# Kernel optimization log

Measured on AMD Instinct MI355X. Metric: run time of the kernel, lower is better.

The kernel has to match this reference:

```python
import jax, jax.numpy as jnp
import numpy as np

K = 512
U = 2
TEMP_BERN = 0.67
TEMP_CAT = 0.67
EULER = 0.5772156649015329
EPS = 1e-8
UEPS = 1e-6


def setup_inputs() -> dict:
    key = jax.random.key(0)
    ks = jax.random.split(key, 3)
    B, D = 16384, 1024
    inputs = jax.random.normal(ks[0], (B, D), jnp.float32)
    # glorot-normal-ish init for mW
    mW = jax.random.normal(ks[1], (D, K * U), jnp.float32) * jnp.sqrt(2.0 / (D + K * U))
    sW = jnp.full((D, K * U), -5.0, jnp.float32)
    conc1 = jnp.full((K,), 2.0, jnp.float32)
    conc0 = jnp.full((K,), 0.5453, jnp.float32)
    t_pi = jax.random.uniform(ks[2], (D, K), jnp.float32, 4.0, 5.0)
    biases = jnp.full((K * U,), 0.1, jnp.float32)
    return {"inputs": inputs, "mW": mW, "sW": sW, "conc1": conc1,
            "conc0": conc0, "t_pi": t_pi, "biases": biases}


def _uniform(k, shape):
    return jax.random.uniform(k, shape, jnp.float32, UEPS, 1.0 - UEPS)


def reference(inputs, mW, sW, conc1, conc0, t_pi, biases):
    rk = jax.random.split(jax.random.key(42), 4)

    # --- reparameterized weights W = mW + eps * softplus(sW) ---
    sW_sp = jax.nn.softplus(sW)
    eps = jax.lax.stop_gradient(jax.random.normal(rk[0], mW.shape, jnp.float32))
    W = mW + eps * sW_sp
    kl_weights = -0.5 * jnp.mean(2.0 * sW_sp - jnp.square(mW) - jnp.square(sW_sp) + 1.0)
    layer_loss = kl_weights / 60000.0

    # --- IBP: relaxed Bernoulli sample of t_pi ([D, K]) ---
    u = _uniform(rk[1], t_pi.shape)
    logistic = jnp.log(u) - jnp.log1p(-u)
    z_sample = jax.nn.sigmoid((t_pi + logistic) / TEMP_BERN)  # bin_concrete_sample
    z = jnp.tile(z_sample, (1, U))  # [D, K*U], column order u*K+k (as in TF code)

    # Kumaraswamy stick-breaking prior: cumprod along axis 0 (TF default)
    a_sp = jax.nn.softplus(conc1)  # [K]
    b_sp = jax.nn.softplus(conc0)  # [K]
    uk = _uniform(rk[2], t_pi.shape)
    q_u = jnp.power(1.0 - jnp.power(uk, 1.0 / b_sp), 1.0 / a_sp)  # kumaraswamy_sample
    prior_pi = jnp.cumprod(q_u, axis=0)
    q = jax.nn.sigmoid(t_pi)
    kl_z = jnp.sum(q * (jnp.log(q + EPS) - jnp.log(prior_pi + EPS)))

    # KL(Kumaraswamy(a,b) || Beta(1,1)); (beta-1) series term vanishes
    kl_sticks = jnp.sum(((a_sp - 1.0) / a_sp) * (-EULER - jax.scipy.special.digamma(b_sp) - 1.0 / b_sp)
                        + jnp.log(a_sp * b_sp + EPS) - (b_sp - 1.0) / b_sp)
    layer_loss = layer_loss + kl_sticks + kl_z

    W = z * W
    out = inputs @ W + biases  # [B, K*U]

    # --- LWTA activation via Gumbel-softmax over U competitors ---
    logits = out.reshape(-1, K, U)  # [B, K, U]
    g = -jnp.log(-jnp.log(_uniform(rk[3], logits.shape)))
    xi = jax.nn.softmax((logits + g) / TEMP_CAT, axis=-1)  # concrete_sample
    out_act = (logits * xi).reshape(out.shape)
    q_xi = jax.nn.softmax(logits, axis=-1)
    kl_xi = jnp.mean(jnp.sum(q_xi * (jnp.log(q_xi + EPS) - jnp.log(1.0 / U)), axis=1))
    layer_loss = layer_loss + kl_xi

    return out_act, layer_loss
```

## Files before the change

kernel.cpp:

```cpp
#include <hip/hip_runtime.h>
#include <stdint.h>
#include <math.h>

#define B_N   16384
#define D_N   1024
#define K_N   512
#define KU_N  1024
#define EPS_F 1e-8f
#define TEMP  0.67f
#define EULERC 0.5772156649015329f

#define HEPS  524288
#define HU    262144
#define HG    8388608

typedef uint32_t u32;
typedef __attribute__((ext_vector_type(4))) float f32x4;
typedef __attribute__((ext_vector_type(8))) __bf16 bf16x8;

#define TF_ROT(x, r) (((x) << (r)) | ((x) >> (32 - (r))))

__host__ __device__ static inline void threefry2x32(u32 k0, u32 k1,
                                                    u32 x0, u32 x1,
                                                    u32* o0, u32* o1) {
  u32 ks2 = k0 ^ k1 ^ 0x1BD11BDAu;
  x0 += k0; x1 += k1;
  x0 += x1; x1 = TF_ROT(x1, 13); x1 ^= x0;
  x0 += x1; x1 = TF_ROT(x1, 15); x1 ^= x0;
  x0 += x1; x1 = TF_ROT(x1, 26); x1 ^= x0;
  x0 += x1; x1 = TF_ROT(x1, 6);  x1 ^= x0;
  x0 += k1; x1 += ks2 + 1u;
  x0 += x1; x1 = TF_ROT(x1, 17); x1 ^= x0;
  x0 += x1; x1 = TF_ROT(x1, 29); x1 ^= x0;
  x0 += x1; x1 = TF_ROT(x1, 16); x1 ^= x0;
  x0 += x1; x1 = TF_ROT(x1, 24); x1 ^= x0;
  x0 += ks2; x1 += k0 + 2u;
  x0 += x1; x1 = TF_ROT(x1, 13); x1 ^= x0;
  x0 += x1; x1 = TF_ROT(x1, 15); x1 ^= x0;
  x0 += x1; x1 = TF_ROT(x1, 26); x1 ^= x0;
  x0 += x1; x1 = TF_ROT(x1, 6);  x1 ^= x0;
  x0 += k0; x1 += k1 + 3u;
  x0 += x1; x1 = TF_ROT(x1, 17); x1 ^= x0;
  x0 += x1; x1 = TF_ROT(x1, 29); x1 ^= x0;
  x0 += x1; x1 = TF_ROT(x1, 16); x1 ^= x0;
  x0 += x1; x1 = TF_ROT(x1, 24); x1 ^= x0;
  x0 += k1; x1 += ks2 + 4u;
  x0 += x1; x1 = TF_ROT(x1, 13); x1 ^= x0;
  x0 += x1; x1 = TF_ROT(x1, 15); x1 ^= x0;
  x0 += x1; x1 = TF_ROT(x1, 26); x1 ^= x0;
  x0 += x1; x1 = TF_ROT(x1, 6);  x1 ^= x0;
  x0 += ks2; x1 += k0 + 5u;
  *o0 = x0; *o1 = x1;
}

__device__ static inline float bits_to_u01(u32 b) {
  u32 f = (b >> 9) | 0x3f800000u;
  return __uint_as_float(f) - 1.0f;
}
__device__ static inline float unif_f(u32 b, float lo, float hi) {
  float f = bits_to_u01(b);
  return fmaxf(lo, f * (hi - lo) + lo);
}
__device__ static inline float erfinv_f(float x) {
  float w = -log1pf(-x * x);
  float p;
  if (w < 5.f) {
    w -= 2.5f;
    p = 2.81022636e-08f;
    p = fmaf(p, w, 3.43273939e-07f);
    p = fmaf(p, w, -3.5233877e-06f);
    p = fmaf(p, w, -4.39150654e-06f);
    p = fmaf(p, w, 0.00021858087f);
    p = fmaf(p, w, -0.00125372503f);
    p = fmaf(p, w, -0.00417768164f);
    p = fmaf(p, w, 0.246640727f);
    p = fmaf(p, w, 1.50140941f);
  } else {
    w = sqrtf(w) - 3.f;
    p = -0.000200214257f;
    p = fmaf(p, w, 0.000100950558f);
    p = fmaf(p, w, 0.00134934322f);
    p = fmaf(p, w, -0.00367342844f);
    p = fmaf(p, w, 0.00573950773f);
    p = fmaf(p, w, -0.0076224613f);
    p = fmaf(p, w, 0.00943887047f);
    p = fmaf(p, w, 1.00167406f);
    p = fmaf(p, w, 2.83297682f);
  }
  return p * x;
}
__device__ static inline float softplus_f(float x) {
  return fmaxf(x, 0.f) + log1pf(expf(-fabsf(x)));
}
__device__ static inline float rcp_f(float x) { return __builtin_amdgcn_rcpf(x); }
__device__ static inline float sigmoid_fast(float x) {
  return rcp_f(1.f + __expf(-x));
}
__device__ static inline float digamma_f(float x) {
  float r = 0.f;
  while (x < 6.f) { r -= 1.f / x; x += 1.f; }
  float inv = 1.f / x, inv2 = inv * inv;
  return r + logf(x) - 0.5f * inv
       - inv2 * (1.f / 12.f - inv2 * (1.f / 120.f - inv2 * (1.f / 252.f)));
}
__device__ static inline unsigned short f2bf_rne(float x) {
  u32 u = __float_as_uint(x);
  u32 r = (u + 0x7fffu + ((u >> 16) & 1u)) >> 16;
  return (unsigned short)r;
}
__device__ static inline u32 cvt_pk_bf16(float lo, float hi) {
  u32 r;
  asm("v_cvt_pk_bf16_f32 %0, %1, %2" : "=v"(r) : "v"(lo), "v"(hi));
  return r;
}
__device__ static inline void gload_lds16(const void* g, void* l) {
  __builtin_amdgcn_global_load_lds(
      (const __attribute__((address_space(1))) u32*)g,
      (__attribute__((address_space(3))) u32*)l, 16, 0, 0);
}

__device__ static inline float block_sum(float v) {
  __shared__ float sm[16];
  int lane = threadIdx.x & 63;
  int wid = threadIdx.x >> 6;
  #pragma unroll
  for (int o = 32; o > 0; o >>= 1) v += __shfl_down(v, o, 64);
  if (lane == 0) sm[wid] = v;
  __syncthreads();
  float s = 0.f;
  if (threadIdx.x == 0) {
    int nw = (blockDim.x + 63) >> 6;
    s = sm[0];
    for (int w = 1; w < nw; ++w) s += sm[w];
  }
  return s;
}

__global__ void k_init(const float* __restrict__ conc1,
                       const float* __restrict__ conc0,
                       float* __restrict__ invA, float* __restrict__ invB,
                       float* gacc) {
  int k = threadIdx.x;
  float a = softplus_f(conc1[k]);
  float b = softplus_f(conc0[k]);
  invA[k] = 1.f / a;
  invB[k] = 1.f / b;
  float s = ((a - 1.f) / a) * (-EULERC - digamma_f(b) - 1.f / b)
          + logf(a * b + EPS_F) - (b - 1.f) / b;
  float t = block_sum(s);
  if (threadIdx.x == 0) { gacc[0] = 0.f; gacc[1] = t; gacc[2] = 0.f; }
}

__global__ __launch_bounds__(256) void k_klz_a(const float* __restrict__ invA,
                                               const float* __restrict__ invB,
                                               float* __restrict__ P,
                                               u32 qk0, u32 qk1) {
  int idx = blockIdx.x * 256 + threadIdx.x;
  int c = idx >> 9, k = idx & (K_N - 1);
  float iA = invA[k], iB = invB[k];
  float p = 1.f;
  int d0 = c << 4;
  for (int d = d0; d < d0 + 16; ++d) {
    int n = (d << 9) + k;
    u32 x0 = (n < HU) ? (u32)n : (u32)(n - HU);
    u32 o0, o1;
    threefry2x32(qk0, qk1, x0, x0 + HU, &o0, &o1);
    u32 bits = (n < HU) ? o0 : o1;
    float u = unif_f(bits, 1e-6f, 1.f - 1e-6f);
    p *= powf(1.f - powf(u, iB), iA);
  }
  P[idx] = p;
}

__global__ __launch_bounds__(256) void k_klz_b(const float* __restrict__ t_pi,
                                               const float* __restrict__ invA,
                                               const float* __restrict__ invB,
                                               const float* __restrict__ P,
                                               float* gacc,
                                               u32 qk0, u32 qk1) {
  int idx = blockIdx.x * 256 + threadIdx.x;
  int c = idx >> 9, k = idx & (K_N - 1);
  float iA = invA[k], iB = invB[k];
  float prior = 1.f;
  for (int c2 = 0; c2 < c; ++c2) prior *= P[(c2 << 9) + k];
  float s = 0.f;
  int d0 = c << 4;
  for (int d = d0; d < d0 + 16; ++d) {
    int n = (d << 9) + k;
    u32 x0 = (n < HU) ? (u32)n : (u32)(n - HU);
    u32 o0, o1;
    threefry2x32(qk0, qk1, x0, x0 + HU, &o0, &o1);
    u32 bits = (n < HU) ? o0 : o1;
    float u = unif_f(bits, 1e-6f, 1.f - 1e-6f);
    prior *= powf(1.f - powf(u, iB), iA);
    float q = sigmoid_fast(t_pi[n]);
    s += q * (__logf(q + EPS_F) - __logf(prior + EPS_F));
  }
  float t = block_sum(s);
  if (threadIdx.x == 0) atomicAdd(&gacc[1], t);
}

__global__ __launch_bounds__(256) void k_wbuildT(const float* __restrict__ mW,
                                                 const float* __restrict__ sW,
                                                 const float* __restrict__ t_pi,
                                                 unsigned short* __restrict__ WzT,
                                                 float* __restrict__ gacc,
                                                 u32 ek0, u32 ek1,
                                                 u32 uk0, u32 uk1) {
  __shared__ unsigned short tile[64][65];
  int dt = (int)blockIdx.x >> 4;
  int jt = (int)blockIdx.x & 15;
  int d0 = dt << 6, j0 = jt << 6;
  int tj = threadIdx.x & 63;
  int tr = threadIdx.x >> 6;
  int j = j0 + tj;
  int kk = j & (K_N - 1);
  bool lowD = (dt < 8);
  float klw = 0.f;
  #pragma unroll 4
  for (int rr = 0; rr < 16; ++rr) {
    int dl = (rr << 2) + tr;
    int d = d0 + dl;
    int n = (d << 10) + j;
    u32 x0 = lowD ? (u32)n : (u32)(n - HEPS);
    u32 o0, o1;
    threefry2x32(ek0, ek1, x0, x0 + HEPS, &o0, &o1);
    u32 ebits = lowD ? o0 : o1;
    int nz = (d << 9) + kk;
    u32 zx0 = lowD ? (u32)nz : (u32)(nz - HU);
    u32 z0, z1;
    threefry2x32(uk0, uk1, zx0, zx0 + HU, &z0, &z1);
    u32 zbits = lowD ? z0 : z1;
    float u = unif_f(zbits, 1e-6f, 1.f - 1e-6f);
    float logistic = __logf(u) - log1pf(-u);
    float z = sigmoid_fast((t_pi[nz] + logistic) * (1.f / TEMP));
    float un = unif_f(ebits, -0.99999994f, 1.0f);
    float epsn = 1.41421356f * erfinv_f(un);
    float m = mW[n], sp = softplus_f(sW[n]);
    tile[tj][dl] = f2bf_rne(z * (m + epsn * sp));
    klw += 2.f * sp - m * m - sp * sp + 1.f;
  }
  __syncthreads();
  #pragma unroll 4
  for (int rr = 0; rr < 16; ++rr) {
    int jl = (rr << 2) + tr;
    WzT[(size_t)(j0 + jl) * D_N + d0 + tj] = tile[jl][tj];
  }
  float t = block_sum(klw);
  if (threadIdx.x == 0) atomicAdd(&gacc[0], t);
}

#define GBM 128
#define GBN 128
#define GBK 32

__global__ __launch_bounds__(256) void k_gemm(const float* __restrict__ A,
                                              const unsigned short* __restrict__ Bt,
                                              const float* __restrict__ bias,
                                              float* __restrict__ C) {
  __shared__ float As[GBM * GBK];
  __shared__ unsigned short Bs[GBN * GBK];

  int f = (int)blockIdx.x;
  int wk = (f & 7) * 128 + (f >> 3);
  const int brow = (wk >> 3) * GBM;
  const int bcol = (wk & 7) * GBN;

  const int tid = threadIdx.x;
  const int lane = tid & 63;
  const int w = tid >> 6;

  const int arr = tid >> 3;
  const int aco = ((tid & 7) ^ (arr & 7)) << 2;
  const float* gA = A + (size_t)(brow + arr) * D_N + aco;
  const int brr = tid >> 2;
  const int bco = ((tid & 3) ^ (brr & 3)) << 3;
  const unsigned short* gB = Bt + (size_t)(bcol + brr) * D_N + bco;

  f32x4 acc[4][4];
  #pragma unroll
  for (int m = 0; m < 4; ++m)
    #pragma unroll
    for (int n = 0; n < 4; ++n) acc[m][n] = (f32x4){0.f, 0.f, 0.f, 0.f};

  const int wr = (w >> 1) << 6;
  const int wc = (w & 1) << 6;
  const int fr = lane & 15;
  const int kg = lane >> 4;

  union BF8 { u32 u[4]; bf16x8 v; };

  for (int kt = 0; kt < D_N; kt += GBK) {
    #pragma unroll
    for (int q = 0; q < 4; ++q)
      gload_lds16(gA + q * (32 * D_N) + kt, (char*)As + q * 4096 + (w << 10));
    #pragma unroll
    for (int q = 0; q < 2; ++q)
      gload_lds16(gB + q * (64 * D_N) + kt, (char*)Bs + q * 4096 + (w << 10));
    __syncthreads();

    BF8 af[4];
    #pragma unroll
    for (int m = 0; m < 4; ++m) {
      int row = wr + m * 16 + fr;
      int r7 = row & 7;
      const float* pa = As + row * GBK;
      f32x4 lov = *(const f32x4*)(pa + ((((kg << 1)    ) ^ r7) << 2));
      f32x4 hiv = *(const f32x4*)(pa + ((((kg << 1) | 1) ^ r7) << 2));
      af[m].u[0] = cvt_pk_bf16(lov.x, lov.y);
      af[m].u[1] = cvt_pk_bf16(lov.z, lov.w);
      af[m].u[2] = cvt_pk_bf16(hiv.x, hiv.y);
      af[m].u[3] = cvt_pk_bf16(hiv.z, hiv.w);
    }
    #pragma unroll
    for (int n = 0; n < 4; ++n) {
      int col = wc + n * 16 + fr;
      bf16x8 bf = *(const bf16x8*)(Bs + col * GBK + ((kg ^ (col & 3)) << 3));
      #pragma unroll
      for (int m = 0; m < 4; ++m)
        acc[m][n] = __builtin_amdgcn_mfma_f32_16x16x32_bf16(af[m].v, bf, acc[m][n], 0, 0, 0);
    }
    __syncthreads();
  }

  #pragma unroll
  for (int n = 0; n < 4; ++n) {
    int col = bcol + wc + n * 16 + fr;
    float bv = bias[col];
    #pragma unroll
    for (int m = 0; m < 4; ++m) {
      int rowb = brow + wr + m * 16 + (kg << 2);
      C[(size_t)(rowb + 0) * KU_N + col] = acc[m][n].x + bv;
      C[(size_t)(rowb + 1) * KU_N + col] = acc[m][n].y + bv;
      C[(size_t)(rowb + 2) * KU_N + col] = acc[m][n].z + bv;
      C[(size_t)(rowb + 3) * KU_N + col] = acc[m][n].w + bv;
    }
  }
}

__device__ static inline float lwta_pair(float v0, float v1, u32 ba, u32 bb,
                                         float* o0, float* o1) {
  float u0 = unif_f(ba, 1e-6f, 1.f - 1e-6f);
  float u1 = unif_f(bb, 1e-6f, 1.f - 1e-6f);
  float g0 = -__logf(-__logf(u0));
  float g1 = -__logf(-__logf(u1));
  const float it = 1.f / TEMP;
  float d = ((v1 + g1) - (v0 + g0)) * it;
  float xi0 = rcp_f(1.f + __expf(d));
  float xi1 = 1.f - xi0;
  *o0 = v0 * xi0;
  *o1 = v1 * xi1;
  float qd = v1 - v0;
  float q0 = rcp_f(1.f + __expf(qd));
  float q1 = 1.f - q0;
  const float LOG2F = 0.6931471805599453f;
  return q0 * (__logf(q0 + EPS_F) + LOG2F) + q1 * (__logf(q1 + EPS_F) + LOG2F);
}

__global__ __launch_bounds__(256) void k_epi(float* __restrict__ C,
                                             float* __restrict__ partial,
                                             u32 gk0, u32 gk1) {
  int idx = blockIdx.x * 256 + threadIdx.x;
  int b = idx >> 9;
  int c2 = (idx & 511) << 1;
  size_t p0 = (size_t)b * KU_N + c2;
  size_t p1 = p0 + (size_t)8192 * KU_N;
  float2 r0 = *(const float2*)&C[p0];
  float2 r1 = *(const float2*)&C[p1];
  u32 m = ((u32)b << 10) | (u32)c2;
  u32 x0a, x1a, x0b, x1b;
  threefry2x32(gk0, gk1, m,      m + HG,      &x0a, &x1a);
  threefry2x32(gk0, gk1, m + 1u, m + 1u + HG, &x0b, &x1b);
  float2 w0, w1;
  float kl = lwta_pair(r0.x, r0.y, x0a, x0b, &w0.x, &w0.y)
           + lwta_pair(r1.x, r1.y, x1a, x1b, &w1.x, &w1.y);
  *(float2*)&C[p0] = w0;
  *(float2*)&C[p1] = w1;
  float t = block_sum(kl);
  if (threadIdx.x == 0) partial[blockIdx.x] = t;
}

#define NPART 16384
__global__ __launch_bounds__(256) void k_final(const float* __restrict__ gacc,
                                               const float* __restrict__ partial,
                                               float* __restrict__ out_loss) {
  float s = 0.f;
  for (int i = threadIdx.x; i < NPART; i += 256) s += partial[i];
  float t = block_sum(s);
  if (threadIdx.x == 0) {
    float kl_weights = -0.5f * (gacc[0] * (1.f / 1048576.f));
    out_loss[0] = kl_weights / 60000.f + gacc[1] + t * (1.f / 32768.f);
  }
}

extern "C" void kernel_launch(void* const* d_in, const int* in_sizes, int n_in,
                              void* d_out, int out_size, void* d_ws, size_t ws_size,
                              hipStream_t stream) {
  (void)in_sizes; (void)n_in; (void)out_size; (void)ws_size;
  const float* inputs = (const float*)d_in[0];
  const float* mW     = (const float*)d_in[1];
  const float* sW     = (const float*)d_in[2];
  const float* conc1  = (const float*)d_in[3];
  const float* conc0  = (const float*)d_in[4];
  const float* t_pi   = (const float*)d_in[5];
  const float* biases = (const float*)d_in[6];
  float* out = (float*)d_out;

  u32 a[4], b[4];
  for (int i = 0; i < 4; ++i)
    threefry2x32(0u, 42u, (u32)i, (u32)(i + 4), &a[i], &b[i]);
  u32 e_k0 = a[0], e_k1 = a[1];
  u32 u_k0 = a[2], u_k1 = a[3];
  u32 q_k0 = b[0], q_k1 = b[1];
  u32 g_k0 = b[2], g_k1 = b[3];

  char* wsb = (char*)d_ws;
  unsigned short* WzT = (unsigned short*)wsb;
  float* P       = (float*)(wsb + (2u << 20));
  float* invA    = (float*)(wsb + (2u << 20) + (128u << 10));
  float* invB    = (float*)(wsb + (2u << 20) + (130u << 10));
  float* gacc    = (float*)(wsb + (2u << 20) + (132u << 10));
  float* partial = (float*)(wsb + (2u << 20) + (136u << 10));

  hipLaunchKernelGGL(k_init, dim3(1), dim3(512), 0, stream,
                     conc1, conc0, invA, invB, gacc);
  hipLaunchKernelGGL(k_klz_a, dim3(128), dim3(256), 0, stream,
                     invA, invB, P, q_k0, q_k1);
  hipLaunchKernelGGL(k_klz_b, dim3(128), dim3(256), 0, stream,
                     t_pi, invA, invB, P, gacc, q_k0, q_k1);
  hipLaunchKernelGGL(k_wbuildT, dim3(256), dim3(256), 0, stream,
                     mW, sW, t_pi, WzT, gacc, e_k0, e_k1, u_k0, u_k1);
  hipLaunchKernelGGL(k_gemm, dim3(1024), dim3(256), 0, stream,
                     inputs, WzT, biases, out);
  hipLaunchKernelGGL(k_epi, dim3(NPART), dim3(256), 0, stream,
                     out, partial, g_k0, g_k1);
  hipLaunchKernelGGL(k_final, dim3(1), dim3(256), 0, stream,
                     gacc, partial, out + 16777216);
}
```

Baseline: 197.5 us.

## Convert A tile to bf16 before LDS and prefetch next A tile in registers

The GEMM now loads the fp32 A tile into registers, converts it to bf16 once per thread, and stores the packed bf16 into a swizzled LDS tile, instead of staging fp32 in LDS and converting per-wave on every fragment read. The next A tile is prefetched into registers while the MFMAs of the current tile run, and the trailing barrier is folded into the loop-top barrier. This halves A's LDS footprint and removes duplicated conversions across waves, at the cost of more registers and synchronous global loads in place of direct-to-LDS loads.

```diff
diff --git a/kernel.cpp b/kernel.cpp
--- a/kernel.cpp
+++ b/kernel.cpp
@@ -16,6 +16,7 @@
 
 typedef uint32_t u32;
 typedef __attribute__((ext_vector_type(4))) float f32x4;
+typedef __attribute__((ext_vector_type(4))) unsigned int u32x4;
 typedef __attribute__((ext_vector_type(8))) __bf16 bf16x8;
 
 #define TF_ROT(x, r) (((x) << (r)) | ((x) >> (32 - (r))))
@@ -258,8 +259,8 @@
                                               const unsigned short* __restrict__ Bt,
                                               const float* __restrict__ bias,
                                               float* __restrict__ C) {
-  __shared__ float As[GBM * GBK];
-  __shared__ unsigned short Bs[GBN * GBK];
+  __shared__ __align__(16) unsigned short As[GBM * GBK];
+  __shared__ __align__(16) unsigned short Bs[GBN * GBK];
 
   int f = (int)blockIdx.x;
   int wk = (f & 7) * 128 + (f >> 3);
@@ -270,9 +271,13 @@
   const int lane = tid & 63;
   const int w = tid >> 6;
 
-  const int arr = tid >> 3;
-  const int aco = ((tid & 7) ^ (arr & 7)) << 2;
-  const float* gA = A + (size_t)(brow + arr) * D_N + aco;
+  const int ar = tid >> 1;
+  const int ac = (tid & 1) << 4;
+  const float* gA = A + (size_t)(brow + ar) * D_N + ac;
+  const int c0 = (tid & 1) << 1;
+  char* asw0 = (char*)As + (ar << 6) + (((c0    ) ^ (ar & 3)) << 4);
+  char* asw1 = (char*)As + (ar << 6) + (((c0 | 1) ^ (ar & 3)) << 4);
+
   const int brr = tid >> 2;
   const int bco = ((tid & 3) ^ (brr & 3)) << 3;
   const unsigned short* gB = Bt + (size_t)(bcol + brr) * D_N + bco;
@@ -288,39 +293,44 @@
   const int fr = lane & 15;
   const int kg = lane >> 4;
 
-  union BF8 { u32 u[4]; bf16x8 v; };
+  f32x4 a0 = *(const f32x4*)(gA + 0);
+  f32x4 a1 = *(const f32x4*)(gA + 4);
+  f32x4 a2 = *(const f32x4*)(gA + 8);
+  f32x4 a3 = *(const f32x4*)(gA + 12);
 
   for (int kt = 0; kt < D_N; kt += GBK) {
-    #pragma unroll
-    for (int q = 0; q < 4; ++q)
-      gload_lds16(gA + q * (32 * D_N) + kt, (char*)As + q * 4096 + (w << 10));
-    #pragma unroll
-    for (int q = 0; q < 2; ++q)
-      gload_lds16(gB + q * (64 * D_N) + kt, (char*)Bs + q * 4096 + (w << 10));
+    u32x4 p0, p1;
+    p0.x = cvt_pk_bf16(a0.x, a0.y); p0.y = cvt_pk_bf16(a0.z, a0.w);
+    p0.z = cvt_pk_bf16(a1.x, a1.y); p0.w = cvt_pk_bf16(a1.z, a1.w);
+    p1.x = cvt_pk_bf16(a2.x, a2.y); p1.y = cvt_pk_bf16(a2.z, a2.w);
+    p1.z = cvt_pk_bf16(a3.x, a3.y); p1.w = cvt_pk_bf16(a3.z, a3.w);
     __syncthreads();
-
-    BF8 af[4];
+    gload_lds16(gB + kt,            (char*)Bs + (w << 10));
+    gload_lds16(gB + 64 * D_N + kt, (char*)Bs + 4096 + (w << 10));
+    *(u32x4*)asw0 = p0;
+    *(u32x4*)asw1 = p1;
+    __syncthreads();
+    if (kt + GBK < D_N) {
+      const float* g = gA + kt + GBK;
+      a0 = *(const f32x4*)(g + 0);
+      a1 = *(const f32x4*)(g + 4);
+      a2 = *(const f32x4*)(g + 8);
+      a3 = *(const f32x4*)(g + 12);
+    }
+    bf16x8 af[4];
     #pragma unroll
     for (int m = 0; m < 4; ++m) {
       int row = wr + m * 16 + fr;
-      int r7 = row & 7;
-      const float* pa = As + row * GBK;
-      f32x4 lov = *(const f32x4*)(pa + ((((kg << 1)    ) ^ r7) << 2));
-      f32x4 hiv = *(const f32x4*)(pa + ((((kg << 1) | 1) ^ r7) << 2));
-      af[m].u[0] = cvt_pk_bf16(lov.x, lov.y);
-      af[m].u[1] = cvt_pk_bf16(lov.z, lov.w);
-      af[m].u[2] = cvt_pk_bf16(hiv.x, hiv.y);
-      af[m].u[3] = cvt_pk_bf16(hiv.z, hiv.w);
+      af[m] = *(const bf16x8*)((char*)As + (row << 6) + ((kg ^ (row & 3)) << 4));
     }
     #pragma unroll
     for (int n = 0; n < 4; ++n) {
       int col = wc + n * 16 + fr;
-      bf16x8 bf = *(const bf16x8*)(Bs + col * GBK + ((kg ^ (col & 3)) << 3));
+      bf16x8 bf = *(const bf16x8*)((char*)Bs + (col << 6) + ((kg ^ (col & 3)) << 4));
       #pragma unroll
       for (int m = 0; m < 4; ++m)
-        acc[m][n] = __builtin_amdgcn_mfma_f32_16x16x32_bf16(af[m].v, bf, acc[m][n], 0, 0, 0);
+        acc[m][n] = __builtin_amdgcn_mfma_f32_16x16x32_bf16(af[m], bf, acc[m][n], 0, 0, 0);
     }
-    __syncthreads();
   }
 
   #pragma unroll
```

New measurement: 190.6 us. 3.5% less time.

## Double-buffer GEMM with register-staged bf16 A tile and K-tile 64

Applied to the files above, without the earlier changes.

Rewrites the GEMM main loop as a double-buffered pipeline over LDS. The fp32 A tile is now loaded into registers and converted to bf16 once, before being stored to LDS, so converted values are reused by every warp instead of being converted again per wave. The B tile is fetched asynchronously into the alternate buffer while MFMAs run on the current one, and GBK doubles to 64 with a new swizzle. This removes one barrier per iteration and halves the A footprint in LDS, at the cost of more registers and hand-written vmcnt waits that must match the number of loads in flight.

```diff
diff --git a/kernel.cpp b/kernel.cpp
--- a/kernel.cpp
+++ b/kernel.cpp
@@ -16,6 +16,7 @@
 
 typedef uint32_t u32;
 typedef __attribute__((ext_vector_type(4))) float f32x4;
+typedef __attribute__((ext_vector_type(4))) unsigned int u32x4;
 typedef __attribute__((ext_vector_type(8))) __bf16 bf16x8;
 
 #define TF_ROT(x, r) (((x) << (r)) | ((x) >> (32 - (r))))
@@ -252,14 +253,14 @@
 
 #define GBM 128
 #define GBN 128
-#define GBK 32
+#define GBK 64
 
 __global__ __launch_bounds__(256) void k_gemm(const float* __restrict__ A,
                                               const unsigned short* __restrict__ Bt,
                                               const float* __restrict__ bias,
                                               float* __restrict__ C) {
-  __shared__ float As[GBM * GBK];
-  __shared__ unsigned short Bs[GBN * GBK];
+  __shared__ __align__(16) unsigned short As[2][GBM * GBK];
+  __shared__ __align__(16) unsigned short Bs[2][GBN * GBK];
 
   int f = (int)blockIdx.x;
   int wk = (f & 7) * 128 + (f >> 3);
@@ -270,12 +271,18 @@
   const int lane = tid & 63;
   const int w = tid >> 6;
 
-  const int arr = tid >> 3;
-  const int aco = ((tid & 7) ^ (arr & 7)) << 2;
-  const float* gA = A + (size_t)(brow + arr) * D_N + aco;
-  const int brr = tid >> 2;
-  const int bco = ((tid & 3) ^ (brr & 3)) << 3;
-  const unsigned short* gB = Bt + (size_t)(bcol + brr) * D_N + bco;
+  const int ar = tid >> 1;
+  const float* gA = A + (size_t)(brow + ar) * D_N + ((tid & 1) << 5);
+  const int cb = (tid & 1) << 2;
+  int aoff[4];
+  #pragma unroll
+  for (int i = 0; i < 4; ++i)
+    aoff[i] = (ar << 7) + (((cb + i) ^ (ar & 7)) << 4);
+
+  const int bcl = tid >> 3;
+  const unsigned short* gB = Bt + (size_t)(bcol + bcl) * D_N
+                           + (((tid & 7) ^ (bcl & 7)) << 3);
+  const int bdst = (w << 10);
 
   f32x4 acc[4][4];
   #pragma unroll
@@ -288,39 +295,100 @@
   const int fr = lane & 15;
   const int kg = lane >> 4;
 
-  union BF8 { u32 u[4]; bf16x8 v; };
-
-  for (int kt = 0; kt < D_N; kt += GBK) {
+  f32x4 av[8];
+
+  #pragma unroll
+  for (int j = 0; j < 8; ++j) av[j] = *(const f32x4*)(gA + (j << 2));
+  #pragma unroll
+  for (int q = 0; q < 4; ++q)
+    gload_lds16(gB + (size_t)(q * 32) * D_N, (char*)Bs[0] + q * 4096 + bdst);
+  __builtin_amdgcn_sched_barrier(0);
+  #pragma unroll
+  for (int i = 0; i < 4; ++i) {
+    u32x4 p;
+    p.x = cvt_pk_bf16(av[2 * i].x, av[2 * i].y);
+    p.y = cvt_pk_bf16(av[2 * i].z, av[2 * i].w);
+    p.z = cvt_pk_bf16(av[2 * i + 1].x, av[2 * i + 1].y);
+    p.w = cvt_pk_bf16(av[2 * i + 1].z, av[2 * i + 1].w);
+    *(u32x4*)((char*)As[0] + aoff[i]) = p;
+  }
+  #pragma unroll
+  for (int j = 0; j < 8; ++j) av[j] = *(const f32x4*)(gA + GBK + (j << 2));
+
+  for (int t = 0; t < 15; ++t) {
+    const int cur = t & 1;
+    char* curA = (char*)As + (cur << 14);
+    char* curB = (char*)Bs + (cur << 14);
+    char* altA = (char*)As + ((cur ^ 1) << 14);
+    char* altB = (char*)Bs + ((cur ^ 1) << 14);
+
+    asm volatile("s_waitcnt vmcnt(8) lgkmcnt(0)" ::: "memory");
+    __builtin_amdgcn_s_barrier();
+
+    {
+      const unsigned short* gBn = gB + ((t + 1) << 6);
+      #pragma unroll
+      for (int q = 0; q < 4; ++q)
+        gload_lds16(gBn + (size_t)(q * 32) * D_N, altB + q * 4096 + bdst);
+    }
+    __builtin_amdgcn_sched_barrier(0);
+
     #pragma unroll
-    for (int q = 0; q < 4; ++q)
-      gload_lds16(gA + q * (32 * D_N) + kt, (char*)As + q * 4096 + (w << 10));
+    for (int h = 0; h < 2; ++h) {
+      bf16x8 af[4];
+      #pragma unroll
+      for (int m = 0; m < 4; ++m) {
+        int row = wr + m * 16 + fr;
+        af[m] = *(const bf16x8*)(curA + (row << 7) + ((((h << 2) + kg) ^ (row & 7)) << 4));
+      }
+      #pragma unroll
+      for (int n = 0; n < 4; ++n) {
+        int col = wc + n * 16 + fr;
+        bf16x8 bf = *(const bf16x8*)(curB + (col << 7) + ((((h << 2) + kg) ^ (col & 7)) << 4));
+        #pragma unroll
+        for (int m = 0; m < 4; ++m)
+          acc[m][n] = __builtin_amdgcn_mfma_f32_16x16x32_bf16(af[m], bf, acc[m][n], 0, 0, 0);
+      }
+    }
+
     #pragma unroll
-    for (int q = 0; q < 2; ++q)
-      gload_lds16(gB + q * (64 * D_N) + kt, (char*)Bs + q * 4096 + (w << 10));
-    __syncthreads();
-
-    BF8 af[4];
+    for (int i = 0; i < 4; ++i) {
+      u32x4 p;
+      p.x = cvt_pk_bf16(av[2 * i].x, av[2 * i].y);
+      p.y = cvt_pk_bf16(av[2 * i].z, av[2 * i].w);
+      p.z = cvt_pk_bf16(av[2 * i + 1].x, av[2 * i + 1].y);
+      p.w = cvt_pk_bf16(av[2 * i + 1].z, av[2 * i + 1].w);
+      *(u32x4*)(altA + aoff[i]) = p;
+    }
+    if (t < 14) {
+      const float* g = gA + ((t + 2) << 6);
+      #pragma unroll
+      for (int j = 0; j < 8; ++j) av[j] = *(const f32x4*)(g + (j << 2));
+    }
+  }
+
+  asm volatile("s_waitcnt vmcnt(0) lgkmcnt(0)" ::: "memory");
+  __builtin_amdgcn_s_barrier();
+  {
+    char* curA = (char*)As + (1 << 14);
+    char* curB = (char*)Bs + (1 << 14);
     #pragma unroll
-    for (int m = 0; m < 4; ++m) {
-      int row = wr + m * 16 + fr;
-      int r7 = row & 7;
-      const float* pa = As + row * GBK;
-      f32x4 lov = *(const f32x4*)(pa + ((((kg << 1)    ) ^ r7) << 2));
-      f32x4 hiv = *(const f32x4*)(pa + ((((kg << 1) | 1) ^ r7) << 2));
-      af[m].u[0] = cvt_pk_bf16(lov.x, lov.y);
-      af[m].u[1] = cvt_pk_bf16(lov.z, lov.w);
-      af[m].u[2] = cvt_pk_bf16(hiv.x, hiv.y);
-      af[m].u[3] = cvt_pk_bf16(hiv.z, hiv.w);
+    for (int h = 0; h < 2; ++h) {
+      bf16x8 af[4];
+      #pragma unroll
+      for (int m = 0; m < 4; ++m) {
+        int row = wr + m * 16 + fr;
+        af[m] = *(const bf16x8*)(curA + (row << 7) + ((((h << 2) + kg) ^ (row & 7)) << 4));
+      }
+      #pragma unroll
+      for (int n = 0; n < 4; ++n) {
+        int col = wc + n * 16 + fr;
+        bf16x8 bf = *(const bf16x8*)(curB + (col << 7) + ((((h << 2) + kg) ^ (col & 7)) << 4));
+        #pragma unroll
+        for (int m = 0; m < 4; ++m)
+          acc[m][n] = __builtin_amdgcn_mfma_f32_16x16x32_bf16(af[m], bf, acc[m][n], 0, 0, 0);
+      }
     }
-    #pragma unroll
-    for (int n = 0; n < 4; ++n) {
-      int col = wc + n * 16 + fr;
-      bf16x8 bf = *(const bf16x8*)(Bs + col * GBK + ((kg ^ (col & 3)) << 3));
-      #pragma unroll
-      for (int m = 0; m < 4; ++m)
-        acc[m][n] = __builtin_amdgcn_mfma_f32_16x16x32_bf16(af[m].v, bf, acc[m][n], 0, 0, 0);
-    }
-    __syncthreads();
   }
 
   #pragma unroll
```

After: 218.0 us. +10.3%, slower.
